# Optimization experiments

Hardware: AMD Instinct MI355X
Metric: run time of the kernel (lower is better)

Reference implementation:

```python
import jax, jax.numpy as jnp
import numpy as np
from jax import lax

DIM = 64
DSTATE = 16
EXPAND = 2
DINNER = DIM * EXPAND
DTRANK = (DIM + 15) // 16  # ceil(d_model/16) = 4
B, D, H, W = 1, 24, 24, 24
EPS = 1e-5


def setup_inputs() -> dict:
    key = jax.random.key(0)
    ks = jax.random.split(key, 40)
    def nrm(i, shape, s=0.02):
        return jax.random.normal(ks[i], shape, jnp.float32) * s
    inp = {}
    inp['x'] = jax.random.normal(ks[0], (B, DIM, D, H, W), jnp.float32)
    # three directional view convs + instance-norm affine params
    inp['w1'] = nrm(1, (DIM, DIM, 3, 1, 1)); inp['b1'] = jnp.zeros((DIM,), jnp.float32)
    inp['g1'] = jnp.ones((DIM,), jnp.float32) + nrm(2, (DIM,)); inp['be1'] = nrm(3, (DIM,))
    inp['w2'] = nrm(4, (DIM, DIM, 1, 3, 1)); inp['b2'] = jnp.zeros((DIM,), jnp.float32)
    inp['g2'] = jnp.ones((DIM,), jnp.float32) + nrm(5, (DIM,)); inp['be2'] = nrm(6, (DIM,))
    inp['w3'] = nrm(7, (DIM, DIM, 1, 1, 3)); inp['b3'] = jnp.zeros((DIM,), jnp.float32)
    inp['g3'] = jnp.ones((DIM,), jnp.float32) + nrm(8, (DIM,)); inp['be3'] = nrm(9, (DIM,))
    # MambaUnit layernorm
    inp['ln_w'] = jnp.ones((DIM,), jnp.float32); inp['ln_b'] = jnp.zeros((DIM,), jnp.float32)
    # Mamba params (shared across the three views, as in the source)
    inp['in_proj_w'] = nrm(10, (2 * DINNER, DIM))
    inp['conv_w'] = jnp.ones((DINNER,), jnp.float32) + nrm(11, (DINNER,))  # d_conv=1 depthwise
    inp['conv_b'] = nrm(12, (DINNER,))
    inp['x_proj_w'] = nrm(13, (DTRANK + 2 * DSTATE, DINNER))
    inp['dt_w'] = nrm(14, (DINNER, DTRANK), 0.1)
    inp['dt_b'] = nrm(15, (DINNER,), 0.1)
    inp['A_log'] = jnp.log(jnp.tile(jnp.arange(1, DSTATE + 1, dtype=jnp.float32), (DINNER, 1)))
    inp['D_param'] = jnp.ones((DINNER,), jnp.float32)
    inp['out_proj_w'] = nrm(16, (DIM, DINNER))
    # fusion 1x1x1 conv + instance norm
    inp['wf'] = nrm(17, (DIM, 3 * DIM, 1, 1, 1)); inp['bf'] = jnp.zeros((DIM,), jnp.float32)
    inp['gf'] = jnp.ones((DIM,), jnp.float32) + nrm(18, (DIM,)); inp['bef'] = nrm(19, (DIM,))
    return inp


def silu(x):
    return x * jax.nn.sigmoid(x)


def conv3d(x, w, b, pad):
    out = lax.conv_general_dilated(
        x, w, (1, 1, 1), [(pad[0], pad[0]), (pad[1], pad[1]), (pad[2], pad[2])],
        dimension_numbers=('NCDHW', 'OIDHW', 'NCDHW'))
    return out + b[None, :, None, None, None]


def instance_norm(x, g, b):
    m = x.mean(axis=(2, 3, 4), keepdims=True)
    v = x.var(axis=(2, 3, 4), keepdims=True)  # biased, as in torch InstanceNorm
    return (x - m) / jnp.sqrt(v + EPS) * g[None, :, None, None, None] + b[None, :, None, None, None]


def layer_norm(x, g, b):
    m = x.mean(axis=-1, keepdims=True)
    v = x.var(axis=-1, keepdims=True)
    return (x - m) / jnp.sqrt(v + EPS) * g + b


def mamba(u, in_proj_w, conv_w, conv_b, x_proj_w, dt_w, dt_b, A_log, D_param, out_proj_w):
    # u: (B, L, d_model)
    xz = u @ in_proj_w.T                       # (B, L, 2*DINNER)
    xi, z = jnp.split(xz, 2, axis=-1)
    xi = silu(xi * conv_w + conv_b)            # d_conv=1 depthwise conv == per-channel affine
    xdbl = xi @ x_proj_w.T                     # (B, L, DTRANK + 2*DSTATE)
    dt = xdbl[..., :DTRANK]
    Bm = xdbl[..., DTRANK:DTRANK + DSTATE]
    Cm = xdbl[..., DTRANK + DSTATE:]
    dt = jax.nn.softplus(dt @ dt_w.T + dt_b)   # (B, L, DINNER)
    A = -jnp.exp(A_log)                        # (DINNER, DSTATE)
    dA = jnp.exp(dt[..., None] * A)            # (B, L, DINNER, DSTATE)
    dBx = dt[..., None] * Bm[:, :, None, :] * xi[..., None]
    def comb(c1, c2):
        a1, b1 = c1
        a2, b2 = c2
        return a1 * a2, a2 * b1 + b2
    _, h = lax.associative_scan(comb, (dA, dBx), axis=1)  # h: (B, L, DINNER, DSTATE)
    y = jnp.einsum('blin,bln->bli', h, Cm) + xi * D_param
    y = y * silu(z)
    return y @ out_proj_w.T


def mamba_unit(x5, ln_w, ln_b, mparams):
    Bb, C = x5.shape[:2]
    dims = x5.shape[2:]
    xf = jnp.transpose(x5.reshape(Bb, C, -1), (0, 2, 1))  # (B, L, C)
    xn = layer_norm(xf, ln_w, ln_b)
    y = mamba(xn, *mparams)
    return jnp.transpose(y, (0, 2, 1)).reshape(Bb, C, *dims)


def reference(x, w1, b1, g1, be1, w2, b2, g2, be2, w3, b3, g3, be3, ln_w, ln_b,
              in_proj_w, conv_w, conv_b, x_proj_w, dt_w, dt_b, A_log, D_param, out_proj_w,
              wf, bf, gf, bef):
    mparams = (in_proj_w, conv_w, conv_b, x_proj_w, dt_w, dt_b, A_log, D_param, out_proj_w)
    v1 = jax.nn.relu(instance_norm(conv3d(x, w1, b1, (1, 0, 0)), g1, be1))
    v2 = jax.nn.relu(instance_norm(conv3d(x, w2, b2, (0, 1, 0)), g2, be2))
    v3 = jax.nn.relu(instance_norm(conv3d(x, w3, b3, (0, 0, 1)), g3, be3))
    m1 = mamba_unit(v1, ln_w, ln_b, mparams)
    m2 = mamba_unit(v2, ln_w, ln_b, mparams)
    m3 = mamba_unit(v3, ln_w, ln_b, mparams)
    cat = jnp.concatenate([m1, m2, m3], axis=1)
    out = jax.nn.relu(instance_norm(conv3d(cat, wf, bf, (0, 0, 0)), gf, bef))
    return out
```

## Files before the change

kernel.cpp:

```cpp
#include <hip/hip_runtime.h>

#define LTOT 13824
#define NCH 108
#define CHL 128
#define EPSF 1e-5f

static const size_t OFF_U   = 1024;
static const size_t NU      = (size_t)3*LTOT*64;
static const size_t NXI     = (size_t)3*LTOT*128;
static const size_t NBM     = (size_t)3*LTOT*16;
static const size_t NAG     = (size_t)3*NCH*128*16;
static const size_t OFF_XIT = OFF_U   + NU;
static const size_t OFF_SZT = OFF_XIT + NXI;
static const size_t OFF_DTT = OFF_SZT + NXI;
static const size_t OFF_BMT = OFF_DTT + NXI;
static const size_t OFF_CMT = OFF_BMT + NBM;
static const size_t OFF_W2  = OFF_CMT + NBM;
static const size_t OFF_WT  = OFF_W2 + 24576;
static const size_t OFF_AGA = OFF_U;
static const size_t OFF_AGB = OFF_U + NAG;
static const size_t OFF_SEED= OFF_U + 2*NAG;
static const size_t OFF_FIN = OFF_DTT;

__device__ __forceinline__ float sigm(float x){ return 1.f/(1.f+__expf(-x)); }
__device__ __forceinline__ float siluf(float x){ return x*sigm(x); }
__device__ __forceinline__ float softplusf(float x){
    return fmaxf(x,0.f) + log1pf(__expf(-fabsf(x)));
}

template<int CTRL>
__device__ __forceinline__ float dpp_add(float x){
    int v = __builtin_amdgcn_update_dpp(0, __float_as_int(x), CTRL, 0xf, 0xf, true);
    return x + __int_as_float(v);
}
__device__ __forceinline__ float sum16(float x){
    x = dpp_add<0xB1>(x);
    x = dpp_add<0x4E>(x);
    x = dpp_add<0x141>(x);
    x = dpp_add<0x140>(x);
    return x;
}

__global__ __launch_bounds__(256) void k_prep(const float* __restrict__ w1,
                      const float* __restrict__ w2, const float* __restrict__ w3,
                      const float* __restrict__ opw, const float* __restrict__ wf,
                      float* __restrict__ wt, float* __restrict__ w2t)
{
    if (blockIdx.x < 144){
        int idx = blockIdx.x*256 + threadIdx.x;
        int r = idx / 12288, rem = idx % 12288;
        int k = rem >> 6, o = rem & 63;
        const float* W = (r==0)?w1:(r==1)?w2:w3;
        wt[idx] = W[o*192 + k];
    } else {
        int idx = (blockIdx.x-144)*256 + threadIdx.x;
        int o = idx & 63, ri = idx >> 6;
        int r = ri >> 7, i = ri & 127;
        float acc = 0.f;
        for (int c2=0;c2<64;c2++)
            acc += opw[c2*128+i] * wf[o*192 + r*64 + c2];
        w2t[idx] = acc;
    }
}

__global__ __launch_bounds__(192) void k_conv(const float* __restrict__ x,
                       const float* __restrict__ wt,
                       const float* __restrict__ b1, const float* __restrict__ b2,
                       const float* __restrict__ b3,
                       float* __restrict__ u, float* __restrict__ ws)
{
    __shared__ __align__(16) float xs[2*1152];
    __shared__ __align__(16) float wl[48*64];
    __shared__ float ssum[64], ssq[64];
    const int r = blockIdx.y;
    const int row0 = blockIdx.x*2;
    const float* Bz = (r==0)?b1:(r==1)?b2:b3;
    const int tid = threadIdx.x;

    if (tid < 64){ ssum[tid]=0.f; ssq[tid]=0.f; }

    const int rw = (tid >= 96) ? 1 : 0, t2 = tid - rw*96;
    const int og = t2 & 15, wg2 = t2 >> 4;
    const int o0 = og*4, w0 = wg2*4;
    float acc[4][4];
    {
        float b0 = Bz[o0], b1v = Bz[o0+1], b2v = Bz[o0+2], b3v = Bz[o0+3];
        #pragma unroll
        for (int wj=0;wj<4;wj++){ acc[0][wj]=b0; acc[1][wj]=b1v; acc[2][wj]=b2v; acc[3][wj]=b3v; }
    }

    const float* wtr = wt + (size_t)r*12288;
    const float* xrow = &xs[rw*1152];
    const int d0 = (row0)/24,   h0 = (row0)%24;
    const int d1 = (row0+1)/24, h1 = (row0+1)%24;

    for (int ph=0; ph<4; ph++){
        __syncthreads();
        for (int s = tid; s < 3072; s += 192)
            wl[s] = wtr[ph*3072 + s];
        for (int rw2=0; rw2<2; rw2++){
            int row = row0 + rw2;
            int d = rw2 ? d1 : d0, h = rw2 ? h1 : h0;
            for (int s = tid; s < 1152; s += 192){
                int w = s % 24; int kt = s / 24; int ic2 = kt/3, t = kt%3;
                int ic = ph*16 + ic2;
                int src = 0; bool valid = true;
                if (r==0){ int dd = d+t-1; valid = (dd>=0 && dd<24); src = (dd*24+h)*24 + w; }
                else if (r==1){ int hh = h+t-1; valid = (hh>=0 && hh<24); src = (d*24+hh)*24 + w; }
                else { int ww = w+t-1; valid = (ww>=0 && ww<24); src = row*24 + ww; }
                xs[rw2*1152 + s] = valid ? x[(size_t)ic*LTOT + src] : 0.f;
            }
        }
        __syncthreads();
        for (int ic2=0; ic2<16; ic2++){
            #pragma unroll
            for (int t=0;t<3;t++){
                float4 wv = *(const float4*)&wl[(ic2*3+t)*64 + o0];
                float4 xv = *(const float4*)&xrow[(ic2*3+t)*24 + w0];
                acc[0][0]=fmaf(wv.x,xv.x,acc[0][0]); acc[0][1]=fmaf(wv.x,xv.y,acc[0][1]);
                acc[0][2]=fmaf(wv.x,xv.z,acc[0][2]); acc[0][3]=fmaf(wv.x,xv.w,acc[0][3]);
                acc[1][0]=fmaf(wv.y,xv.x,acc[1][0]); acc[1][1]=fmaf(wv.y,xv.y,acc[1][1]);
                acc[1][2]=fmaf(wv.y,xv.z,acc[1][2]); acc[1][3]=fmaf(wv.y,xv.w,acc[1][3]);
                acc[2][0]=fmaf(wv.z,xv.x,acc[2][0]); acc[2][1]=fmaf(wv.z,xv.y,acc[2][1]);
                acc[2][2]=fmaf(wv.z,xv.z,acc[2][2]); acc[2][3]=fmaf(wv.z,xv.w,acc[2][3]);
                acc[3][0]=fmaf(wv.w,xv.x,acc[3][0]); acc[3][1]=fmaf(wv.w,xv.y,acc[3][1]);
                acc[3][2]=fmaf(wv.w,xv.z,acc[3][2]); acc[3][3]=fmaf(wv.w,xv.w,acc[3][3]);
            }
        }
    }

    size_t ub = ((size_t)r*LTOT + (size_t)(row0+rw)*24)*64;
    float ps[4]={0,0,0,0}, pq[4]={0,0,0,0};
    #pragma unroll
    for (int wj=0; wj<4; wj++){
        float4 v = make_float4(acc[0][wj],acc[1][wj],acc[2][wj],acc[3][wj]);
        *(float4*)&u[ub + (size_t)(w0+wj)*64 + o0] = v;
        ps[0]+=v.x; pq[0]+=v.x*v.x; ps[1]+=v.y; pq[1]+=v.y*v.y;
        ps[2]+=v.z; pq[2]+=v.z*v.z; ps[3]+=v.w; pq[3]+=v.w*v.w;
    }
    #pragma unroll
    for (int oj=0;oj<4;oj++){
        atomicAdd(&ssum[o0+oj], ps[oj]);
        atomicAdd(&ssq[o0+oj], pq[oj]);
    }
    __syncthreads();
    if (tid < 64){
        atomicAdd(&ws[r*64 + tid], ssum[tid]);
        atomicAdd(&ws[192 + r*64 + tid], ssq[tid]);
    }
}

__global__ __launch_bounds__(192) void k_stats1(float* ws){
    int t = threadIdx.x;
    float s = ws[t], q = ws[192+t];
    float m = s*(1.f/(float)LTOT);
    float v = q*(1.f/(float)LTOT) - m*m;
    ws[512+t] = m; ws[704+t] = rsqrtf(v + EPSF);
}

__global__ __launch_bounds__(256) void k_inproj(const float* __restrict__ u, float* __restrict__ xiT,
                         float* __restrict__ szT, const float* __restrict__ ipw,
                         const float* __restrict__ cw, const float* __restrict__ cb,
                         const float* __restrict__ ws,
                         const float* g1,const float* be1,const float* g2,const float* be2,
                         const float* g3,const float* be3,
                         const float* lnw,const float* lnb)
{
    __shared__ __align__(16) float xl[32*64];
    __shared__ float xo[32*257];
    const int tid = threadIdx.x, r = blockIdx.y;
    const int wv = tid >> 6, lane = tid & 63;
    const int l0 = blockIdx.x*32;
    size_t gbase = (size_t)r*LTOT + l0;

    float wr[64];
    const float4* wp = (const float4*)(ipw + (size_t)tid*64);
    #pragma unroll
    for (int q=0;q<16;q++){
        float4 u4 = wp[q];
        wr[4*q]=u4.x; wr[4*q+1]=u4.y; wr[4*q+2]=u4.z; wr[4*q+3]=u4.w;
    }

    {
        const float* g  = (r==0)?g1:(r==1)?g2:g3;
        const float* be = (r==0)?be1:(r==1)?be2:be3;
        float m  = ws[512 + r*64 + lane], rs = ws[704 + r*64 + lane];
        float gg = g[lane], bb = be[lane];
        float lw = lnw[lane], lb = lnb[lane];
        for (int j=0;j<8;j++){
            int p = 4*j + wv;
            float vv = u[(gbase+p)*64 + lane];
            vv = fmaxf((vv-m)*rs*gg + bb, 0.f);
            float s1 = sum16(vv), s2 = sum16(vv*vv);
            s1 += __shfl_xor(s1,16); s2 += __shfl_xor(s2,16);
            s1 += __shfl_xor(s1,32); s2 += __shfl_xor(s2,32);
            float mean = s1*(1.f/64.f);
            float var  = s2*(1.f/64.f) - mean*mean;
            xl[p*64 + lane] = (vv-mean)*rsqrtf(var+EPSF)*lw + lb;
        }
    }
    const bool isx = tid < 128;
    float ccw=0.f, ccb=0.f;
    if (isx){ ccw = cw[tid]; ccb = cb[tid]; }
    __syncthreads();

    #pragma unroll 4
    for (int p=0;p<32;p++){
        const float4* xp = (const float4*)&xl[p*64];
        float a0=0,a1=0,a2=0,a3=0;
        #pragma unroll
        for (int q=0;q<16;q++){
            float4 a = xp[q];
            a0=fmaf(wr[4*q],a.x,a0); a1=fmaf(wr[4*q+1],a.y,a1);
            a2=fmaf(wr[4*q+2],a.z,a2); a3=fmaf(wr[4*q+3],a.w,a3);
        }
        float acc = (a0+a1)+(a2+a3);
        float v = isx ? siluf(fmaf(acc, ccw, ccb)) : siluf(acc);
        xo[p*257 + tid] = v;
    }
    __syncthreads();

    for (int s = tid; s < 2048; s += 256){
        int ch = s >> 3, q = s & 7;
        float4 v = make_float4(xo[(q*4+0)*257+ch], xo[(q*4+1)*257+ch],
                               xo[(q*4+2)*257+ch], xo[(q*4+3)*257+ch]);
        float* dst = (ch < 128) ? xiT : szT;
        int c2 = ch & 127;
        *(float4*)&dst[((size_t)r*128 + c2)*LTOT + l0 + q*4] = v;
    }
}

__global__ __launch_bounds__(256) void k_xproj(const float* __restrict__ xiT, float* __restrict__ dtT,
                        float* __restrict__ BmT, float* __restrict__ CmT,
                        const float* __restrict__ xpw, const float* __restrict__ dtw,
                        const float* __restrict__ dtb)
{
    __shared__ __align__(16) float xt[128*36];
    __shared__ float ww[36*129];
    __shared__ float sd[4*36];
    const int tid = threadIdx.x, r = blockIdx.y;
    const int l0 = blockIdx.x*32;

    for (int s = tid; s < 4096; s += 256){
        int c = s>>5, p = s&31;
        xt[c*36+p] = xiT[((size_t)r*128 + c)*LTOT + l0 + p];
    }
    for (int s = tid; s < 4608; s += 256){
        int k = s>>7, c = s&127;
        ww[k*129+c] = xpw[s];
    }
    __syncthreads();

    const int wv = tid>>6, lane = tid&63;
    float acc[8] = {0,0,0,0,0,0,0,0};
    if (lane < 36){
        const float* wrow = &ww[lane*129];
        for (int c=0;c<128;c++){
            float w = wrow[c];
            float4 a = *(const float4*)&xt[c*36 + wv*8];
            float4 b = *(const float4*)&xt[c*36 + wv*8 + 4];
            acc[0]=fmaf(w,a.x,acc[0]); acc[1]=fmaf(w,a.y,acc[1]);
            acc[2]=fmaf(w,a.z,acc[2]); acc[3]=fmaf(w,a.w,acc[3]);
            acc[4]=fmaf(w,b.x,acc[4]); acc[5]=fmaf(w,b.y,acc[5]);
            acc[6]=fmaf(w,b.z,acc[6]); acc[7]=fmaf(w,b.w,acc[7]);
        }
    }
    if (lane>=4 && lane<36){
        float* dst = (lane<20) ? BmT : CmT;
        int n = (lane<20) ? (lane-4) : (lane-20);
        size_t base = ((size_t)r*16 + n)*LTOT + l0 + wv*8;
        *(float4*)&dst[base]   = make_float4(acc[0],acc[1],acc[2],acc[3]);
        *(float4*)&dst[base+4] = make_float4(acc[4],acc[5],acc[6],acc[7]);
    }
    if (lane < 4){
        #pragma unroll
        for (int p=0;p<8;p++) sd[lane*36 + wv*8 + p] = acc[p];
    }
    __syncthreads();

    const int i = tid>>1, ph = tid&1;
    float4 dw = *(const float4*)&dtw[i*4];
    float db = dtb[i];
    float buf[16];
    #pragma unroll
    for (int t=0;t<16;t++){
        int p = ph*16 + t;
        float v = db + dw.x*sd[0*36+p] + dw.y*sd[1*36+p]
                     + dw.z*sd[2*36+p] + dw.w*sd[3*36+p];
        buf[t] = softplusf(v);
    }
    size_t base = ((size_t)r*128 + i)*LTOT + l0 + ph*16;
    #pragma unroll
    for (int q=0;q<4;q++){
        *(float4*)&dtT[base + 4*q] =
            make_float4(buf[4*q], buf[4*q+1], buf[4*q+2], buf[4*q+3]);
    }
}

__global__ __launch_bounds__(256) void k_scan1(const float* __restrict__ dtT, const float* __restrict__ BmT,
                        const float* __restrict__ xiT, const float* __restrict__ Alog,
                        float* __restrict__ aga, float* __restrict__ agb)
{
    __shared__ float4 sdt[16*33], sxi[16*33], sbm[16*33];
    const int tid = threadIdx.x;
    const int n = tid & 15, il = tid >> 4;
    const int c = blockIdx.x, ib = blockIdx.y, r = blockIdx.z;
    const int i = ib*16 + il;

    for (int f = tid; f < 512; f += 256){
        int ii = f >> 5, t4 = f & 31;
        size_t rowI = ((size_t)r*128 + ib*16 + ii)*LTOT + (size_t)c*CHL + t4*4;
        size_t rowN = ((size_t)r*16  + ii)*LTOT + (size_t)c*CHL + t4*4;
        sdt[ii*33 + t4] = *(const float4*)&dtT[rowI];
        sxi[ii*33 + t4] = *(const float4*)&xiT[rowI];
        sbm[ii*33 + t4] = *(const float4*)&BmT[rowN];
    }
    __syncthreads();

    const float A2 = -expf(Alog[i*16+n]) * 1.44269504f;
    float b = 0.f, sdtacc = 0.f;
    #define S1_STEP(dv,xv,bv) { float e=exp2f(A2*(dv)); b=fmaf(e,b,(dv)*(xv)*(bv)); }
    for (int t4 = 0; t4 < 32; t4++){
        float4 d = sdt[il*33 + t4];
        float4 x = sxi[il*33 + t4];
        float4 m = sbm[n*33 + t4];
        sdtacc += ((d.x+d.y)+(d.z+d.w));
        S1_STEP(d.x,x.x,m.x) S1_STEP(d.y,x.y,m.y)
        S1_STEP(d.z,x.z,m.z) S1_STEP(d.w,x.w,m.w)
    }
    size_t o = ((size_t)(r*NCH+c)*128 + i)*16 + n;
    aga[o] = exp2f(A2*sdtacc);
    agb[o] = b;
}

__global__ __launch_bounds__(512) void k_scan2(const float* __restrict__ aga, const float* __restrict__ agb,
                        float* __restrict__ seed)
{
    int t = blockIdx.x*512 + threadIdx.x;
    int r = t >> 11, rem = t & 2047;
    float h = 0.f;
    for (int c=0;c<NCH;c++){
        size_t idx = (size_t)(r*NCH+c)*2048 + rem;
        float a = aga[idx], b = agb[idx];
        seed[idx] = h;
        h = fmaf(a, h, b);
    }
}

__global__ __launch_bounds__(256) void k_scan3(const float* __restrict__ dtT, const float* __restrict__ BmT,
                        const float* __restrict__ CmT, const float* __restrict__ xiT,
                        float* __restrict__ szT, const float* __restrict__ Alog,
                        const float* __restrict__ Dp, const float* __restrict__ seed)
{
    __shared__ float4 sdt[16*33], sxi[16*33], sbm[16*33], scm[16*33];
    const int tid = threadIdx.x;
    const int n = tid & 15, il = tid >> 4;
    const int c = blockIdx.x, ib = blockIdx.y, r = blockIdx.z;
    const int i = ib*16 + il;

    for (int f = tid; f < 512; f += 256){
        int ii = f >> 5, t4 = f & 31;
        size_t rowI = ((size_t)r*128 + ib*16 + ii)*LTOT + (size_t)c*CHL + t4*4;
        size_t rowN = ((size_t)r*16  + ii)*LTOT + (size_t)c*CHL + t4*4;
        sdt[ii*33 + t4] = *(const float4*)&dtT[rowI];
        sxi[ii*33 + t4] = *(const float4*)&xiT[rowI];
        sbm[ii*33 + t4] = *(const float4*)&BmT[rowN];
        scm[ii*33 + t4] = *(const float4*)&CmT[rowN];
    }
    __syncthreads();

    const float A2 = -expf(Alog[i*16+n]) * 1.44269504f;
    const float Dv = Dp[i];
    float h = seed[(size_t)(r*NCH+c)*2048 + (i*16+n)];

    #define S3_STEP(dv,xv,bv,cv,oyv) { \
        float e=exp2f(A2*(dv)); h=fmaf(e,h,(dv)*(xv)*(bv)); \
        float py=sum16(h*(cv)); oyv = fmaf((xv),Dv,py); }
    for (int t4 = 0; t4 < 32; t4++){
        float4 d = sdt[il*33 + t4];
        float4 x = sxi[il*33 + t4];
        float4 m = sbm[n*33 + t4];
        float4 cv = scm[n*33 + t4];
        float4 yv;
        S3_STEP(d.x,x.x,m.x,cv.x, yv.x)
        S3_STEP(d.y,x.y,m.y,cv.y, yv.y)
        S3_STEP(d.z,x.z,m.z,cv.z, yv.z)
        S3_STEP(d.w,x.w,m.w,cv.w, yv.w)
        if (n==0) sdt[il*33 + t4] = yv;
    }
    __syncthreads();

    for (int f = tid; f < 512; f += 256){
        int ii = f >> 5, t4 = f & 31;
        size_t rowI = ((size_t)r*128 + ib*16 + ii)*LTOT + (size_t)c*CHL + t4*4;
        float4 yv = sdt[ii*33 + t4];
        float4 s  = *(const float4*)&szT[rowI];
        *(float4*)&szT[rowI] = make_float4(yv.x*s.x, yv.y*s.y, yv.z*s.z, yv.w*s.w);
    }
}

__global__ __launch_bounds__(256, 1) void k_fin(const float* __restrict__ yT, const float* __restrict__ w2t,
                      const float* __restrict__ bfb, float* __restrict__ fin,
                      float* __restrict__ ws)
{
    __shared__ __align__(16) float yl[384*20];
    __shared__ float part[4*16*64];
    __shared__ float ssum[64], ssq[64];
    const int tid = threadIdx.x;
    const int l0 = blockIdx.x*16;
    const int o = tid & 63, sg = tid >> 6;

    for (int f = tid; f < 6144; f += 256){
        int k = f >> 4, p = f & 15;
        yl[k*20 + p] = yT[(size_t)k*LTOT + l0 + p];
    }
    float wreg[96];
    {
        const float* wp = w2t + (size_t)(sg*96)*64 + o;
        #pragma unroll
        for (int j=0;j<96;j++) wreg[j] = wp[(size_t)j*64];
    }
    if (tid < 64){ ssum[tid]=0.f; ssq[tid]=0.f; }
    __syncthreads();

    float acc[16];
    #pragma unroll
    for (int p=0;p<16;p++) acc[p]=0.f;
    const float* ylbase = &yl[sg*96*20];
    #pragma unroll
    for (int j=0;j<96;j++){
        float w = wreg[j];
        const float4* yp4 = (const float4*)&ylbase[j*20];
        float4 a = yp4[0], b = yp4[1], c = yp4[2], d = yp4[3];
        acc[0] =fmaf(w,a.x,acc[0]);  acc[1] =fmaf(w,a.y,acc[1]);
        acc[2] =fmaf(w,a.z,acc[2]);  acc[3] =fmaf(w,a.w,acc[3]);
        acc[4] =fmaf(w,b.x,acc[4]);  acc[5] =fmaf(w,b.y,acc[5]);
        acc[6] =fmaf(w,b.z,acc[6]);  acc[7] =fmaf(w,b.w,acc[7]);
        acc[8] =fmaf(w,c.x,acc[8]);  acc[9] =fmaf(w,c.y,acc[9]);
        acc[10]=fmaf(w,c.z,acc[10]); acc[11]=fmaf(w,c.w,acc[11]);
        acc[12]=fmaf(w,d.x,acc[12]); acc[13]=fmaf(w,d.y,acc[13]);
        acc[14]=fmaf(w,d.z,acc[14]); acc[15]=fmaf(w,d.w,acc[15]);
    }
    #pragma unroll
    for (int p=0;p<16;p++) part[(sg*16+p)*64 + o] = acc[p];
    __syncthreads();

    float bias = bfb[o];
    float ps=0.f, pq=0.f;
    #pragma unroll
    for (int j=0;j<4;j++){
        int p = sg + j*4;
        float s = part[(0*16+p)*64+o] + part[(1*16+p)*64+o]
                + part[(2*16+p)*64+o] + part[(3*16+p)*64+o] + bias;
        fin[(size_t)(l0+p)*64 + o] = s;
        ps += s; pq += s*s;
    }
    atomicAdd(&ssum[o], ps); atomicAdd(&ssq[o], pq);
    __syncthreads();
    if (tid<64){
        atomicAdd(&ws[384+tid], ssum[tid]);
        atomicAdd(&ws[448+tid], ssq[tid]);
    }
}

__global__ __launch_bounds__(64) void k_statsF(float* ws){
    int t = threadIdx.x;
    float s = ws[384+t], q = ws[448+t];
    float m = s*(1.f/(float)LTOT);
    float v = q*(1.f/(float)LTOT) - m*m;
    ws[896+t] = m; ws[960+t] = rsqrtf(v + EPSF);
}

__global__ __launch_bounds__(256) void k_out(const float* __restrict__ fin, const float* __restrict__ ws,
                      const float* __restrict__ gf, const float* __restrict__ bef,
                      float* __restrict__ out)
{
    __shared__ float tl[64*65];
    const int tid = threadIdx.x;
    const int l0 = blockIdx.x*64;
    for (int s=tid; s<4096; s+=256){
        int li = s>>6, o = s&63;
        float v = fin[(size_t)(l0+li)*64 + o];
        v = fmaxf((v - ws[896+o])*ws[960+o]*gf[o] + bef[o], 0.f);
        tl[o*65+li] = v;
    }
    __syncthreads();
    for (int s=tid; s<4096; s+=256){
        int o = s>>6, li = s&63;
        out[(size_t)o*LTOT + l0 + li] = tl[o*65+li];
    }
}

extern "C" void kernel_launch(void* const* d_in, const int* in_sizes, int n_in,
                              void* d_out, int out_size, void* d_ws, size_t ws_size,
                              hipStream_t stream)
{
    const float* X    = (const float*)d_in[0];
    const float* W1   = (const float*)d_in[1];  const float* B1  = (const float*)d_in[2];
    const float* G1   = (const float*)d_in[3];  const float* BE1 = (const float*)d_in[4];
    const float* W2   = (const float*)d_in[5];  const float* B2  = (const float*)d_in[6];
    const float* G2   = (const float*)d_in[7];  const float* BE2 = (const float*)d_in[8];
    const float* W3   = (const float*)d_in[9];  const float* B3  = (const float*)d_in[10];
    const float* G3   = (const float*)d_in[11]; const float* BE3 = (const float*)d_in[12];
    const float* LNW  = (const float*)d_in[13]; const float* LNB = (const float*)d_in[14];
    const float* IPW  = (const float*)d_in[15];
    const float* CW   = (const float*)d_in[16]; const float* CB  = (const float*)d_in[17];
    const float* XPW  = (const float*)d_in[18];
    const float* DTW  = (const float*)d_in[19]; const float* DTB = (const float*)d_in[20];
    const float* ALOG = (const float*)d_in[21]; const float* DP  = (const float*)d_in[22];
    const float* OPW  = (const float*)d_in[23];
    const float* WF   = (const float*)d_in[24]; const float* BF  = (const float*)d_in[25];
    const float* GF   = (const float*)d_in[26]; const float* BEF = (const float*)d_in[27];
    float* ws = (float*)d_ws;

    (void)hipMemsetAsync(d_ws, 0, 2048, stream);

    k_prep  <<<240, 256, 0, stream>>>(W1, W2, W3, OPW, WF, ws+OFF_WT, ws+OFF_W2);
    k_conv  <<<dim3(288,3), 192, 0, stream>>>(X, ws+OFF_WT, B1, B2, B3, ws+OFF_U, ws);
    k_stats1<<<1, 192, 0, stream>>>(ws);
    k_inproj<<<dim3(432,3), 256, 0, stream>>>(ws+OFF_U, ws+OFF_XIT, ws+OFF_SZT,
                                              IPW, CW, CB, ws,
                                              G1,BE1,G2,BE2,G3,BE3, LNW,LNB);
    k_xproj <<<dim3(432,3), 256, 0, stream>>>(ws+OFF_XIT, ws+OFF_DTT, ws+OFF_BMT,
                                              ws+OFF_CMT, XPW, DTW, DTB);
    k_scan1 <<<dim3(NCH,8,3), 256, 0, stream>>>(ws+OFF_DTT, ws+OFF_BMT, ws+OFF_XIT,
                                                ALOG, ws+OFF_AGA, ws+OFF_AGB);
    k_scan2 <<<12, 512, 0, stream>>>(ws+OFF_AGA, ws+OFF_AGB, ws+OFF_SEED);
    k_scan3 <<<dim3(NCH,8,3), 256, 0, stream>>>(ws+OFF_DTT, ws+OFF_BMT, ws+OFF_CMT,
                                                ws+OFF_XIT, ws+OFF_SZT, ALOG, DP,
                                                ws+OFF_SEED);
    k_fin   <<<864, 256, 0, stream>>>(ws+OFF_SZT, ws+OFF_W2, BF, ws+OFF_FIN, ws);
    k_statsF<<<1, 64, 0, stream>>>(ws);
    k_out   <<<216, 256, 0, stream>>>(ws+OFF_FIN, ws, GF, BEF, (float*)d_out);
}
```

Before: 396.9 us.

## Restructure in_proj: wave-uniform transposed weights, 64-position tiles, direct coalesced stores

The in_proj kernel now gives each wave 64 output channels and each lane one sequence position. Weights come from a pre-transposed copy made in k_prep and are read at wave-uniform addresses, which allows scalar loads. This replaces the 64-register per-thread weight rows and the extra shared-memory staging and transpose used for output. Each block covers 64 positions instead of 32, and results are written directly as coalesced stores along L. The trade-off is a 64-float accumulator array per thread, which raises register pressure under the new launch bound.

```diff
diff --git a/kernel.cpp b/kernel.cpp
--- a/kernel.cpp
+++ b/kernel.cpp
@@ -17,6 +17,7 @@
 static const size_t OFF_CMT = OFF_BMT + NBM;
 static const size_t OFF_W2  = OFF_CMT + NBM;
 static const size_t OFF_WT  = OFF_W2 + 24576;
+static const size_t OFF_WI  = OFF_WT + 36864;
 static const size_t OFF_AGA = OFF_U;
 static const size_t OFF_AGB = OFF_U + NAG;
 static const size_t OFF_SEED= OFF_U + 2*NAG;
@@ -44,7 +45,9 @@
 __global__ __launch_bounds__(256) void k_prep(const float* __restrict__ w1,
                       const float* __restrict__ w2, const float* __restrict__ w3,
                       const float* __restrict__ opw, const float* __restrict__ wf,
-                      float* __restrict__ wt, float* __restrict__ w2t)
+                      const float* __restrict__ ipw,
+                      float* __restrict__ wt, float* __restrict__ w2t,
+                      float* __restrict__ wi)
 {
     if (blockIdx.x < 144){
         int idx = blockIdx.x*256 + threadIdx.x;
@@ -52,7 +55,7 @@
         int k = rem >> 6, o = rem & 63;
         const float* W = (r==0)?w1:(r==1)?w2:w3;
         wt[idx] = W[o*192 + k];
-    } else {
+    } else if (blockIdx.x < 240){
         int idx = (blockIdx.x-144)*256 + threadIdx.x;
         int o = idx & 63, ri = idx >> 6;
         int r = ri >> 7, i = ri & 127;
@@ -60,6 +63,10 @@
         for (int c2=0;c2<64;c2++)
             acc += opw[c2*128+i] * wf[o*192 + r*64 + c2];
         w2t[idx] = acc;
+    } else {
+        int idx = (blockIdx.x-240)*256 + threadIdx.x;
+        int col = idx & 255, q = idx >> 8;
+        wi[q*256 + col] = ipw[col*64 + q];
     }
 }
 
@@ -158,28 +165,20 @@
     ws[512+t] = m; ws[704+t] = rsqrtf(v + EPSF);
 }
 
-__global__ __launch_bounds__(256) void k_inproj(const float* __restrict__ u, float* __restrict__ xiT,
-                         float* __restrict__ szT, const float* __restrict__ ipw,
+__global__ __launch_bounds__(256, 4) void k_inproj(const float* __restrict__ u, float* __restrict__ xiT,
+                         float* __restrict__ szT, const float* __restrict__ wi,
                          const float* __restrict__ cw, const float* __restrict__ cb,
                          const float* __restrict__ ws,
                          const float* g1,const float* be1,const float* g2,const float* be2,
                          const float* g3,const float* be3,
                          const float* lnw,const float* lnb)
 {
-    __shared__ __align__(16) float xl[32*64];
-    __shared__ float xo[32*257];
+    __shared__ float xl[64*65];
     const int tid = threadIdx.x, r = blockIdx.y;
-    const int wv = tid >> 6, lane = tid & 63;
-    const int l0 = blockIdx.x*32;
+    const int lane = tid & 63;
+    const int wv = __builtin_amdgcn_readfirstlane(tid >> 6);
+    const int l0 = blockIdx.x*64;
     size_t gbase = (size_t)r*LTOT + l0;
-
-    float wr[64];
-    const float4* wp = (const float4*)(ipw + (size_t)tid*64);
-    #pragma unroll
-    for (int q=0;q<16;q++){
-        float4 u4 = wp[q];
-        wr[4*q]=u4.x; wr[4*q+1]=u4.y; wr[4*q+2]=u4.z; wr[4*q+3]=u4.w;
-    }
 
     {
         const float* g  = (r==0)?g1:(r==1)?g2:g3;
@@ -187,8 +186,8 @@
         float m  = ws[512 + r*64 + lane], rs = ws[704 + r*64 + lane];
         float gg = g[lane], bb = be[lane];
         float lw = lnw[lane], lb = lnb[lane];
-        for (int j=0;j<8;j++){
-            int p = 4*j + wv;
+        for (int j=0;j<16;j++){
+            int p = wv*16 + j;
             float vv = u[(gbase+p)*64 + lane];
             vv = fmaxf((vv-m)*rs*gg + bb, 0.f);
             float s1 = sum16(vv), s2 = sum16(vv*vv);
@@ -196,37 +195,33 @@
             s1 += __shfl_xor(s1,32); s2 += __shfl_xor(s2,32);
             float mean = s1*(1.f/64.f);
             float var  = s2*(1.f/64.f) - mean*mean;
-            xl[p*64 + lane] = (vv-mean)*rsqrtf(var+EPSF)*lw + lb;
+            xl[lane*65 + p] = (vv-mean)*rsqrtf(var+EPSF)*lw + lb;
         }
     }
-    const bool isx = tid < 128;
-    float ccw=0.f, ccb=0.f;
-    if (isx){ ccw = cw[tid]; ccb = cb[tid]; }
-    __syncthreads();
-
-    #pragma unroll 4
-    for (int p=0;p<32;p++){
-        const float4* xp = (const float4*)&xl[p*64];
-        float a0=0,a1=0,a2=0,a3=0;
+    __syncthreads();
+
+    float acc[64];
+    #pragma unroll
+    for (int j=0;j<64;j++) acc[j] = 0.f;
+    const float* wbase = wi + wv*64;
+    for (int q=0;q<64;q++){
+        float xq = xl[q*65 + lane];
+        const float* wq = wbase + q*256;
         #pragma unroll
-        for (int q=0;q<16;q++){
-            float4 a = xp[q];
-            a0=fmaf(wr[4*q],a.x,a0); a1=fmaf(wr[4*q+1],a.y,a1);
-            a2=fmaf(wr[4*q+2],a.z,a2); a3=fmaf(wr[4*q+3],a.w,a3);
-        }
-        float acc = (a0+a1)+(a2+a3);
-        float v = isx ? siluf(fmaf(acc, ccw, ccb)) : siluf(acc);
-        xo[p*257 + tid] = v;
-    }
-    __syncthreads();
-
-    for (int s = tid; s < 2048; s += 256){
-        int ch = s >> 3, q = s & 7;
-        float4 v = make_float4(xo[(q*4+0)*257+ch], xo[(q*4+1)*257+ch],
-                               xo[(q*4+2)*257+ch], xo[(q*4+3)*257+ch]);
-        float* dst = (ch < 128) ? xiT : szT;
-        int c2 = ch & 127;
-        *(float4*)&dst[((size_t)r*128 + c2)*LTOT + l0 + q*4] = v;
+        for (int j=0;j<64;j++)
+            acc[j] = fmaf(wq[j], xq, acc[j]);
+    }
+
+    const bool isx = (wv < 2);
+    float* dst = isx ? xiT : szT;
+    const int c0 = (wv & 1)*64;
+    #pragma unroll
+    for (int j=0;j<64;j++){
+        int c2 = c0 + j;
+        float v;
+        if (isx) v = siluf(fmaf(acc[j], cw[c2], cb[c2]));
+        else     v = siluf(acc[j]);
+        dst[((size_t)r*128 + c2)*LTOT + l0 + lane] = v;
     }
 }
 
@@ -515,11 +510,12 @@
 
     (void)hipMemsetAsync(d_ws, 0, 2048, stream);
 
-    k_prep  <<<240, 256, 0, stream>>>(W1, W2, W3, OPW, WF, ws+OFF_WT, ws+OFF_W2);
+    k_prep  <<<304, 256, 0, stream>>>(W1, W2, W3, OPW, WF, IPW,
+                                      ws+OFF_WT, ws+OFF_W2, ws+OFF_WI);
     k_conv  <<<dim3(288,3), 192, 0, stream>>>(X, ws+OFF_WT, B1, B2, B3, ws+OFF_U, ws);
     k_stats1<<<1, 192, 0, stream>>>(ws);
-    k_inproj<<<dim3(432,3), 256, 0, stream>>>(ws+OFF_U, ws+OFF_XIT, ws+OFF_SZT,
-                                              IPW, CW, CB, ws,
+    k_inproj<<<dim3(216,3), 256, 0, stream>>>(ws+OFF_U, ws+OFF_XIT, ws+OFF_SZT,
+                                              ws+OFF_WI, CW, CB, ws,
                                               G1,BE1,G2,BE2,G3,BE3, LNW,LNB);
     k_xproj <<<dim3(432,3), 256, 0, stream>>>(ws+OFF_XIT, ws+OFF_DTT, ws+OFF_BMT,
                                               ws+OFF_CMT, XPW, DTW, DTB);
```

Result: faster. 372.4 us, median of 2 (-6.2%).
